# Performance work log

Hardware: AMD Instinct MI355X
Metric: run time of the kernel (lower is better)

The kernel has to match this reference:

```python
import jax, jax.numpy as jnp
import numpy as np

N0, N1, N2 = 100000, 400000, 100000
EU0, EU1, EB1, EB2 = 1600000, 1200000, 800000, 300000
D, H = 64, 64  # layer_dim, hidden
BN_EPS = 1e-5


def _bn(x, g, b):
    # BatchNorm1d in training mode (batch statistics, biased variance)
    m = jnp.mean(x, axis=0)
    v = jnp.mean((x - m) ** 2, axis=0)
    return (x - m) * jax.lax.rsqrt(v + BN_EPS) * g + b


def _mlp(x, W1, b1, g1, be1, W2, b2, g2, be2):
    # Linear -> BN -> ReLU -> Linear -> BN -> ReLU
    h = jax.nn.relu(_bn(x @ W1 + b1, g1, be1))
    return jax.nn.relu(_bn(h @ W2 + b2, g2, be2))


def setup_inputs() -> dict:
    key = jax.random.key(0)
    ks = jax.random.split(key, 16)
    s = 0.1  # weight init scale
    inp = {
        'x0': jax.random.normal(ks[0], (N0, D), jnp.float32),
        'x1': jax.random.normal(ks[1], (N1, D), jnp.float32),
        'x2': jax.random.normal(ks[2], (N2, D), jnp.float32),
        'up_index0': jax.random.randint(ks[3], (2, EU0), 0, N0, jnp.int32),
        'up_index1': jax.random.randint(ks[4], (2, EU1), 0, N1, jnp.int32),
        'bnd_src1': jax.random.randint(ks[5], (EB1,), 0, N0, jnp.int32),
        'bnd_dst1': jax.random.randint(ks[6], (EB1,), 0, N1, jnp.int32),
        'bnd_src2': jax.random.randint(ks[7], (EB2,), 0, N1, jnp.int32),
        'bnd_dst2': jax.random.randint(ks[8], (EB2,), 0, N2, jnp.int32),
        'up_W1': jax.random.normal(ks[9], (3, D, H), jnp.float32) * s,
        'up_b1': jnp.zeros((3, H), jnp.float32),
        'up_g1': jnp.ones((3, H), jnp.float32),
        'up_be1': jnp.zeros((3, H), jnp.float32),
        'up_W2': jax.random.normal(ks[10], (3, H, H), jnp.float32) * s,
        'up_b2': jnp.zeros((3, H), jnp.float32),
        'up_g2': jnp.ones((3, H), jnp.float32),
        'up_be2': jnp.zeros((3, H), jnp.float32),
        'bd_W1': jax.random.normal(ks[11], (3, D, H), jnp.float32) * s,
        'bd_b1': jnp.zeros((3, H), jnp.float32),
        'bd_g1': jnp.ones((3, H), jnp.float32),
        'bd_be1': jnp.zeros((3, H), jnp.float32),
        'bd_W2': jax.random.normal(ks[12], (3, H, H), jnp.float32) * s,
        'bd_b2': jnp.zeros((3, H), jnp.float32),
        'bd_g2': jnp.ones((3, H), jnp.float32),
        'bd_be2': jnp.zeros((3, H), jnp.float32),
        'cmb_W': jax.random.normal(ks[13], (3, 2 * H, H), jnp.float32) * s,
        'cmb_b': jnp.zeros((3, H), jnp.float32),
        'cmb_g': jnp.ones((3, H), jnp.float32),
        'cmb_be': jnp.zeros((3, H), jnp.float32),
        'eps': jnp.zeros((3,), jnp.float32),  # eps1 per dim (eps2 unused in forward)
    }
    return inp


def reference(x0, x1, x2, up_index0, up_index1, bnd_src1, bnd_dst1, bnd_src2, bnd_dst2,
              up_W1, up_b1, up_g1, up_be1, up_W2, up_b2, up_g2, up_be2,
              bd_W1, bd_b1, bd_g1, bd_be1, bd_W2, bd_b2, bd_g2, bd_be2,
              cmb_W, cmb_b, cmb_g, cmb_be, eps):
    seg = jax.ops.segment_sum

    def level(d, x, agg_up, agg_bd):
        z = (1.0 + eps[d]) * x
        out_up = _mlp(agg_up + z, up_W1[d], up_b1[d], up_g1[d], up_be1[d],
                      up_W2[d], up_b2[d], up_g2[d], up_be2[d])
        out_bd = _mlp(agg_bd + z, bd_W1[d], bd_b1[d], bd_g1[d], bd_be1[d],
                      bd_W2[d], bd_b2[d], bd_g2[d], bd_be2[d])
        cat = jnp.concatenate([out_up, out_bd], axis=-1)
        return jax.nn.relu(_bn(cat @ cmb_W[d] + cmb_b[d], cmb_g[d], cmb_be[d]))

    # dim 0: upper adjacency only (no boundaries for nodes)
    agg_up0 = seg(x0[up_index0[0]], up_index0[1], num_segments=N0)
    out0 = level(0, x0, agg_up0, jnp.zeros_like(x0))

    # dim 1: upper adjacency (via 2-cells) + node boundaries (boundary_attr = x0)
    agg_up1 = seg(x1[up_index1[0]], up_index1[1], num_segments=N1)
    agg_bd1 = seg(x0[bnd_src1], bnd_dst1, num_segments=N1)
    out1 = level(1, x1, agg_up1, agg_bd1)

    # dim 2: edge boundaries only (boundary_attr = x1), no upper adjacency
    agg_bd2 = seg(x1[bnd_src2], bnd_dst2, num_segments=N2)
    out2 = level(2, x2, jnp.zeros_like(x2), agg_bd2)

    return (out0, out1, out2)
```

## Files before the change

kernel.cpp:

```cpp
#include <hip/hip_runtime.h>
#include <cstdint>
#include <cstddef>


using bfrag = __attribute__((ext_vector_type(8))) short;
using f32x4 = __attribute__((ext_vector_type(4))) float;

__device__ __forceinline__ unsigned short f2bf(float f) {
    unsigned int u = __float_as_uint(f);
    u += 0x7FFFu + ((u >> 16) & 1u);
    return (unsigned short)(u >> 16);
}
__device__ __forceinline__ float bf2f(unsigned int h) {
    return __uint_as_float(h << 16);
}


__global__ __launch_bounds__(256) void hist_ranged_k(
    const int* __restrict__ d0, const int* __restrict__ d1,
    const int* __restrict__ d2, const int* __restrict__ d3,
    int E0, int E1, int E2, int E3,
    int o0, int o1, int o2, int o3,
    int* __restrict__ cnt, int NT)
{
    const int pass = blockIdx.x & 7;
    const int W = (NT + 7) >> 3;
    const int lo = pass * W;
    int hi = lo + W; if (hi > NT) hi = NT;
    const int ET = E0 + E1 + E2 + E3;
    const int nsub = gridDim.x >> 3;
    for (int e = (blockIdx.x >> 3) * 256 + threadIdx.x; e < ET; e += nsub * 256) {
        int g;
        if (e < E0) g = o0 + d0[e];
        else if (e < E0 + E1) g = o1 + d1[e - E0];
        else if (e < E0 + E1 + E2) g = o2 + d2[e - E0 - E1];
        else g = o3 + d3[e - E0 - E1 - E2];
        if (g >= lo && g < hi) atomicAdd(&cnt[g], 1);
    }
}

__global__ __launch_bounds__(256) void fill_ranged_k(
    const int* __restrict__ s0, const int* __restrict__ d0,
    const int* __restrict__ s1, const int* __restrict__ d1,
    const int* __restrict__ s2, const int* __restrict__ d2,
    const int* __restrict__ s3, const int* __restrict__ d3,
    int E0, int E1, int E2, int E3,
    int o0, int o1, int o2, int o3,
    int* __restrict__ cur, int* __restrict__ esrc, int NT)
{
    const int pass = blockIdx.x & 7;
    const int W = (NT + 7) >> 3;
    const int lo = pass * W;
    int hi = lo + W; if (hi > NT) hi = NT;
    const int ET = E0 + E1 + E2 + E3;
    const int nsub = gridDim.x >> 3;
    for (int e = (blockIdx.x >> 3) * 256 + threadIdx.x; e < ET; e += nsub * 256) {
        int g; const int* sp; int ei;
        if (e < E0) { g = o0 + d0[e]; sp = s0; ei = e; }
        else if (e < E0 + E1) { ei = e - E0; g = o1 + d1[ei]; sp = s1; }
        else if (e < E0 + E1 + E2) { ei = e - E0 - E1; g = o2 + d2[ei]; sp = s2; }
        else { ei = e - E0 - E1 - E2; g = o3 + d3[ei]; sp = s3; }
        if (g >= lo && g < hi) {
            int pos = atomicAdd(&cur[g], 1);
            esrc[pos] = sp[ei];
        }
    }
}

__global__ __launch_bounds__(256) void scanA_k(int* __restrict__ a,
                                               int* __restrict__ bsum, int n) {
    __shared__ int ts[256];
    int tid = threadIdx.x;
    int base = blockIdx.x * 2048 + tid * 8;
    int v[8]; int s = 0;
    #pragma unroll
    for (int i = 0; i < 8; ++i) { v[i] = (base + i < n) ? a[base + i] : 0; s += v[i]; }
    ts[tid] = s;
    __syncthreads();
    for (int off = 1; off < 256; off <<= 1) {
        int t = (tid >= off) ? ts[tid - off] : 0;
        __syncthreads();
        ts[tid] += t;
        __syncthreads();
    }
    int run = ts[tid] - s;
    #pragma unroll
    for (int i = 0; i < 8; ++i) {
        if (base + i < n) { int o = v[i]; a[base + i] = run; run += o; }
    }
    if (tid == 255) bsum[blockIdx.x] = ts[255];
}

__global__ __launch_bounds__(512) void scanB_k(int* __restrict__ bsum, int nb) {
    __shared__ int ls[512];
    int tid = threadIdx.x;
    int v = (tid < nb) ? bsum[tid] : 0;
    ls[tid] = v;
    __syncthreads();
    for (int off = 1; off < 512; off <<= 1) {
        int t = (tid >= off) ? ls[tid - off] : 0;
        __syncthreads();
        ls[tid] += t;
        __syncthreads();
    }
    if (tid < nb) bsum[tid] = ls[tid] - v;
}

__global__ __launch_bounds__(256) void scanC_k(int* __restrict__ a,
                                               const int* __restrict__ bsum, int n) {
    int base = blockIdx.x * 2048 + threadIdx.x * 8;
    int add = bsum[blockIdx.x];
    #pragma unroll
    for (int i = 0; i < 8; ++i)
        if (base + i < n) a[base + i] += add;
}


__global__ __launch_bounds__(256) void wprep_k(
    const float* __restrict__ upW1, const float* __restrict__ upW2,
    const float* __restrict__ bdW1, const float* __restrict__ bdW2,
    const float* __restrict__ cmbW, unsigned short* __restrict__ wT)
{
    int id = blockIdx.x;
    int d = id / 5, j = id % 5;
    const float* src; int K = 64;
    if (j == 0)      src = upW1 + (size_t)d * 4096;
    else if (j == 1) src = upW2 + (size_t)d * 4096;
    else if (j == 2) src = bdW1 + (size_t)d * 4096;
    else if (j == 3) src = bdW2 + (size_t)d * 4096;
    else           { src = cmbW + (size_t)d * 8192; K = 128; }
    unsigned short* dst = wT + (size_t)d * 24576 + (j < 4 ? j * 4096 : 16384);
    for (int e = threadIdx.x; e < K * 64; e += 256) {
        int k = e >> 6, n = e & 63;
        dst[n * K + k] = f2bf(src[e]);
    }
}


struct SegG {
    const int* cur;
    const float* xs; const float* xself;
    const unsigned short* in0; const unsigned short* in1;
    const float* st0; const float* g0; const float* be0;
    const float* st1; const float* g1; const float* be1;
    const unsigned short* wT; const float* bias;
    unsigned short* out; float* ostats;
    int N; int blk0; int eBase; int epsIdx;
};
struct GemmArgs { SegG s[6]; int nseg; const int* esrc; const float* epsP; };

__global__ __launch_bounds__(256) void gemm_bn_multi_k(int mode, GemmArgs A)
{
    __shared__ unsigned short sIn[64][72];
    __shared__ unsigned short sW[64][72];
    __shared__ float sCoef[4][64];
    __shared__ float sBias[64];
    __shared__ float sRedS[4][64];
    __shared__ float sRedQ[4][64];

    int si = 0;
    #pragma unroll
    for (int i = 1; i < 6; ++i)
        if (i < A.nseg && (int)blockIdx.x >= A.s[i].blk0) si = i;
    const SegG S = A.s[si];
    const int* esrc = A.esrc;

    const int tid = threadIdx.x;
    const int row0 = ((int)blockIdx.x - S.blk0) * 64;
    const int N = S.N;
    const float Nf = (float)N;

    if (tid < 64) {
        sBias[tid] = S.bias[tid];
        if (mode >= 1) {
            float s = S.st0[tid], sq = S.st0[64 + tid];
            float m = s / Nf, v = sq / Nf - m * m;
            float a = S.g0[tid] * rsqrtf(v + 1e-5f);
            sCoef[0][tid] = a; sCoef[1][tid] = S.be0[tid] - a * m;
        }
    } else if (tid < 128 && mode == 2) {
        int k = tid - 64;
        float s = S.st1[k], sq = S.st1[64 + k];
        float m = s / Nf, v = sq / Nf - m * m;
        float a = S.g1[k] * rsqrtf(v + 1e-5f);
        sCoef[2][k] = a; sCoef[3][k] = S.be1[k] - a * m;
    }
    const float sx = (mode == 0) ? (1.0f + A.epsP[S.epsIdx]) : 0.f;
    __syncthreads();

    f32x4 acc[4] = {};
    const int K = (mode == 2) ? 128 : 64;
    const int nch = (mode == 2) ? 2 : 1;
    const int wv = tid >> 6, l = tid & 63, l15 = l & 15, quad = l >> 4;

    for (int ch = 0; ch < nch; ++ch) {
        if (ch) __syncthreads();
        if (mode == 0) {
            const int grp = tid >> 4, lane = tid & 15;
            const int r0g = row0 + grp * 4;
            float ax[4], ay[4], az[4], aw[4];
            int beg[4], deg[4];
            #pragma unroll
            for (int rr = 0; rr < 4; ++rr) {
                int gr = r0g + rr;
                float4 xv = {0.f, 0.f, 0.f, 0.f};
                if (gr < N)
                    xv = *(const float4*)(S.xself + (size_t)gr * 64 + lane * 4);
                ax[rr] = sx * xv.x; ay[rr] = sx * xv.y;
                az[rr] = sx * xv.z; aw[rr] = sx * xv.w;
                int b = 0, d = 0;
                if (gr < N && S.cur) {
                    b = (gr == 0) ? S.eBase : S.cur[gr - 1];
                    d = S.cur[gr] - b;
                }
                beg[rr] = b; deg[rr] = d;
            }
            #pragma unroll
            for (int rr = 0; rr < 4; ++rr) {
                for (int base = 0; base < deg[rr]; base += 16) {
                    int take = deg[rr] - base; if (take > 16) take = 16;
                    int idxl = 0;
                    if (lane < take) idxl = esrc[beg[rr] + base + lane];
                    for (int j0 = 0; j0 < take; j0 += 4) {
                        float4 v0 = {0,0,0,0}, v1 = {0,0,0,0};
                        float4 v2 = {0,0,0,0}, v3 = {0,0,0,0};
                        int si2 = __shfl(idxl, j0, 16);
                        v0 = *(const float4*)(S.xs + (size_t)si2 * 64 + lane * 4);
                        if (j0 + 1 < take) {
                            si2 = __shfl(idxl, j0 + 1, 16);
                            v1 = *(const float4*)(S.xs + (size_t)si2 * 64 + lane * 4);
                        }
                        if (j0 + 2 < take) {
                            si2 = __shfl(idxl, j0 + 2, 16);
                            v2 = *(const float4*)(S.xs + (size_t)si2 * 64 + lane * 4);
                        }
                        if (j0 + 3 < take) {
                            si2 = __shfl(idxl, j0 + 3, 16);
                            v3 = *(const float4*)(S.xs + (size_t)si2 * 64 + lane * 4);
                        }
                        ax[rr] += (v0.x + v1.x) + (v2.x + v3.x);
                        ay[rr] += (v0.y + v1.y) + (v2.y + v3.y);
                        az[rr] += (v0.z + v1.z) + (v2.z + v3.z);
                        aw[rr] += (v0.w + v1.w) + (v2.w + v3.w);
                    }
                }
                ushort4 pk;
                pk.x = f2bf(ax[rr]); pk.y = f2bf(ay[rr]);
                pk.z = f2bf(az[rr]); pk.w = f2bf(aw[rr]);
                *(ushort4*)&sIn[grp * 4 + rr][lane * 4] = pk;
            }
        } else {
            const unsigned short* base = ch ? S.in1 : S.in0;
            const int ci = ch * 2;
            #pragma unroll
            for (int it = 0; it < 2; ++it) {
                int id = tid + it * 256;
                int r = id >> 3, c8 = id & 7;
                int gr = row0 + r;
                uint4 pk = {0u, 0u, 0u, 0u};
                if (gr < N) {
                    uint4 raw = *(const uint4*)(base + (size_t)gr * 64 + c8 * 8);
                    unsigned int rw[4] = {raw.x, raw.y, raw.z, raw.w};
                    unsigned int ow[4];
                    #pragma unroll
                    for (int q2 = 0; q2 < 4; ++q2) {
                        int col = c8 * 8 + q2 * 2;
                        float v0 = fmaxf(fmaf(sCoef[ci][col], bf2f(rw[q2] & 0xFFFFu),
                                              sCoef[ci + 1][col]), 0.f);
                        float v1 = fmaxf(fmaf(sCoef[ci][col + 1], bf2f(rw[q2] >> 16),
                                              sCoef[ci + 1][col + 1]), 0.f);
                        ow[q2] = (unsigned int)f2bf(v0) | ((unsigned int)f2bf(v1) << 16);
                    }
                    pk.x = ow[0]; pk.y = ow[1]; pk.z = ow[2]; pk.w = ow[3];
                }
                *(uint4*)&sIn[r][c8 * 8] = pk;
            }
        }
        #pragma unroll
        for (int it = 0; it < 2; ++it) {
            int id = tid + it * 256;
            int nr = id >> 3, c8 = id & 7;
            uint4 w = *(const uint4*)(S.wT + (size_t)nr * K + ch * 64 + c8 * 8);
            *(uint4*)&sW[nr][c8 * 8] = w;
        }
        __syncthreads();
        bfrag a0 = *(const bfrag*)&sIn[16 * wv + l15][quad * 8];
        bfrag a1 = *(const bfrag*)&sIn[16 * wv + l15][32 + quad * 8];
        #pragma unroll
        for (int c = 0; c < 4; ++c) {
            bfrag b0 = *(const bfrag*)&sW[16 * c + l15][quad * 8];
            bfrag b1 = *(const bfrag*)&sW[16 * c + l15][32 + quad * 8];
            acc[c] = __builtin_amdgcn_mfma_f32_16x16x32_bf16(a0, b0, acc[c], 0, 0, 0);
            acc[c] = __builtin_amdgcn_mfma_f32_16x16x32_bf16(a1, b1, acc[c], 0, 0, 0);
        }
    }

    float psv[4], pqv[4];
    #pragma unroll
    for (int c = 0; c < 4; ++c) {
        int col = 16 * c + l15;
        float b = sBias[col];
        float ps = 0.f, pq = 0.f;
        #pragma unroll
        for (int r = 0; r < 4; ++r) {
            int grow = row0 + 16 * wv + quad * 4 + r;
            if (grow < N) {
                float v = acc[c][r] + b;
                S.out[(size_t)grow * 64 + col] = f2bf(v);
                ps += v; pq += v * v;
            }
        }
        psv[c] = ps; pqv[c] = pq;
    }
    #pragma unroll
    for (int c = 0; c < 4; ++c) {
        float ps = psv[c], pq = pqv[c];
        ps += __shfl_xor(ps, 16, 64); pq += __shfl_xor(pq, 16, 64);
        ps += __shfl_xor(ps, 32, 64); pq += __shfl_xor(pq, 32, 64);
        if (l < 16) { sRedS[wv][16 * c + l] = ps; sRedQ[wv][16 * c + l] = pq; }
    }
    __syncthreads();
    if (tid < 64) {
        float s = sRedS[0][tid] + sRedS[1][tid] + sRedS[2][tid] + sRedS[3][tid];
        float q = sRedQ[0][tid] + sRedQ[1][tid] + sRedQ[2][tid] + sRedQ[3][tid];
        unsafeAtomicAdd(&S.ostats[tid], s);
        unsafeAtomicAdd(&S.ostats[64 + tid], q);
    }
}


struct SegA {
    const unsigned short* in; const float* st; const float* g; const float* be;
    float* out; int N; int blk0;
};
struct ApplyArgs { SegA s[2]; int nseg; };

__global__ __launch_bounds__(256) void bn_relu_apply_multi_k(ApplyArgs A)
{
    __shared__ float sa[64], sc[64];
    int si = 0;
    if (A.nseg > 1 && (int)blockIdx.x >= A.s[1].blk0) si = 1;
    const SegA S = A.s[si];
    int tid = threadIdx.x;
    if (tid < 64) {
        float s = S.st[tid], sq = S.st[64 + tid];
        float m = s / (float)S.N, v = sq / (float)S.N - m * m;
        float a = S.g[tid] * rsqrtf(v + 1e-5f);
        sa[tid] = a; sc[tid] = S.be[tid] - a * m;
    }
    __syncthreads();
    int idx = ((int)blockIdx.x - S.blk0) * 256 + tid;
    if (idx < S.N * 8) {
        int r = idx >> 3, c8 = idx & 7;
        uint4 raw = *(const uint4*)(S.in + (size_t)r * 64 + c8 * 8);
        unsigned int rw[4] = {raw.x, raw.y, raw.z, raw.w};
        float o[8];
        #pragma unroll
        for (int q = 0; q < 4; ++q) {
            int col = c8 * 8 + q * 2;
            o[q * 2 + 0] = fmaxf(fmaf(sa[col + 0], bf2f(rw[q] & 0xFFFFu), sc[col + 0]), 0.f);
            o[q * 2 + 1] = fmaxf(fmaf(sa[col + 1], bf2f(rw[q] >> 16), sc[col + 1]), 0.f);
        }
        float4 o0 = {o[0], o[1], o[2], o[3]}, o1 = {o[4], o[5], o[6], o[7]};
        *(float4*)(S.out + (size_t)r * 64 + c8 * 8) = o0;
        *(float4*)(S.out + (size_t)r * 64 + c8 * 8 + 4) = o1;
    }
}

extern "C" void kernel_launch(void* const* d_in, const int* in_sizes, int n_in,
                              void* d_out, int out_size, void* d_ws, size_t ws_size,
                              hipStream_t stream) {
    (void)n_in; (void)out_size; (void)ws_size;
    const float* x0 = (const float*)d_in[0];
    const float* x1 = (const float*)d_in[1];
    const float* x2 = (const float*)d_in[2];
    const int* up_index0 = (const int*)d_in[3];
    const int* up_index1 = (const int*)d_in[4];
    const int* bnd_src1  = (const int*)d_in[5];
    const int* bnd_dst1  = (const int*)d_in[6];
    const int* bnd_src2  = (const int*)d_in[7];
    const int* bnd_dst2  = (const int*)d_in[8];
    const float* up_W1 = (const float*)d_in[9];
    const float* up_b1 = (const float*)d_in[10];
    const float* up_g1 = (const float*)d_in[11];
    const float* up_be1= (const float*)d_in[12];
    const float* up_W2 = (const float*)d_in[13];
    const float* up_b2 = (const float*)d_in[14];
    const float* up_g2 = (const float*)d_in[15];
    const float* up_be2= (const float*)d_in[16];
    const float* bd_W1 = (const float*)d_in[17];
    const float* bd_b1 = (const float*)d_in[18];
    const float* bd_g1 = (const float*)d_in[19];
    const float* bd_be1= (const float*)d_in[20];
    const float* bd_W2 = (const float*)d_in[21];
    const float* bd_b2 = (const float*)d_in[22];
    const float* bd_g2 = (const float*)d_in[23];
    const float* bd_be2= (const float*)d_in[24];
    const float* cmb_W = (const float*)d_in[25];
    const float* cmb_b = (const float*)d_in[26];
    const float* cmb_g = (const float*)d_in[27];
    const float* cmb_be= (const float*)d_in[28];
    const float* epsP  = (const float*)d_in[29];

    const int EU0 = in_sizes[3] / 2, EU1 = in_sizes[4] / 2;
    const int EB1 = in_sizes[5],     EB2 = in_sizes[7];
    const int n0 = in_sizes[0] / 64, n1 = in_sizes[1] / 64, n2 = in_sizes[2] / 64;
    const int nMax02 = (n0 > n2) ? n0 : n2;

    float* outP = (float*)d_out;

    unsigned short* bufU = (unsigned short*)d_ws;
    unsigned short* bufB = bufU + (size_t)n1 * 64;
    float* stats = (float*)(bufB + (size_t)nMax02 * 64);
    int*   bsum  = (int*)(stats + 15 * 128);
    unsigned short* wT = (unsigned short*)(bsum + 1024);

    const int NT  = n0 + 2 * n1 + n2;
    const int ETT = EU0 + EU1 + EB1 + EB2;
    const int oU0 = 0, oU1 = n0, oB1 = n0 + n1, oB2 = n0 + 2 * n1;
    const int eU0 = 0, eU1 = EU0, eB1 = EU0 + EU1, eB2 = EU0 + EU1 + EB1;
    int* curAll  = (int*)(outP + (size_t)(n0 + n1) * 64);
    int* esrcAll = curAll + NT;

    unsigned short* hU0 = bufB;
    unsigned short* hB0 = (unsigned short*)outP;
    unsigned short* hU2 = (unsigned short*)outP + (size_t)n0 * 64;
    unsigned short* hU1 = bufU;
    unsigned short* hB1 = (unsigned short*)(outP + (size_t)n0 * 64);
    unsigned short* hB2 = (unsigned short*)(outP + (size_t)n0 * 64) + (size_t)n1 * 64;

    hipMemsetAsync(stats, 0, 15 * 128 * sizeof(float), stream);
    wprep_k<<<15, 256, 0, stream>>>(up_W1, up_W2, bd_W1, bd_W2, cmb_W, wT);

    hipMemsetAsync(curAll, 0, (size_t)NT * sizeof(int), stream);
    hist_ranged_k<<<2048, 256, 0, stream>>>(
        up_index0 + EU0, up_index1 + EU1, bnd_dst1, bnd_dst2,
        EU0, EU1, EB1, EB2, oU0, oU1, oB1, oB2, curAll, NT);
    int nbScan = (NT + 2047) / 2048;
    scanA_k<<<nbScan, 256, 0, stream>>>(curAll, bsum, NT);
    scanB_k<<<1, 512, 0, stream>>>(bsum, nbScan);
    scanC_k<<<nbScan, 256, 0, stream>>>(curAll, bsum, NT);
    fill_ranged_k<<<2048, 256, 0, stream>>>(
        up_index0, up_index0 + EU0, up_index1, up_index1 + EU1,
        bnd_src1, bnd_dst1, bnd_src2, bnd_dst2,
        EU0, EU1, EB1, EB2, oU0, oU1, oB1, oB2, curAll, esrcAll, NT);

    auto S  = [&](int d, int i) { return stats + (size_t)(d * 5 + i) * 128; };
    auto WTf = [&](int d, int j) { return wT + (size_t)d * 24576 + (j < 4 ? j * 4096 : 16384); };

    const int nb0 = (n0 + 63) / 64, nb1 = (n1 + 63) / 64, nb2 = (n2 + 63) / 64;

    {
        GemmArgs A{}; A.nseg = 6; A.esrc = esrcAll; A.epsP = epsP;
        auto& s = A.s;
        s[0] = { curAll + oU0, x0, x0, nullptr, nullptr,
                 nullptr, nullptr, nullptr, nullptr, nullptr, nullptr,
                 WTf(0,0), up_b1 + 0, hU0, S(0,0), n0, 0, eU0, 0 };
        s[1] = { nullptr, nullptr, x0, nullptr, nullptr,
                 nullptr, nullptr, nullptr, nullptr, nullptr, nullptr,
                 WTf(0,2), bd_b1 + 0, hB0, S(0,2), n0, nb0, 0, 0 };
        s[2] = { curAll + oU1, x1, x1, nullptr, nullptr,
                 nullptr, nullptr, nullptr, nullptr, nullptr, nullptr,
                 WTf(1,0), up_b1 + 64, hU1, S(1,0), n1, 2*nb0, eU1, 1 };
        s[3] = { curAll + oB1, x0, x1, nullptr, nullptr,
                 nullptr, nullptr, nullptr, nullptr, nullptr, nullptr,
                 WTf(1,2), bd_b1 + 64, hB1, S(1,2), n1, 2*nb0 + nb1, eB1, 1 };
        s[4] = { nullptr, nullptr, x2, nullptr, nullptr,
                 nullptr, nullptr, nullptr, nullptr, nullptr, nullptr,
                 WTf(2,0), up_b1 + 128, hU2, S(2,0), n2, 2*nb0 + 2*nb1, 0, 2 };
        s[5] = { curAll + oB2, x1, x2, nullptr, nullptr,
                 nullptr, nullptr, nullptr, nullptr, nullptr, nullptr,
                 WTf(2,2), bd_b1 + 128, hB2, S(2,2), n2, 2*nb0 + 2*nb1 + nb2, eB2, 2 };
        gemm_bn_multi_k<<<2*nb0 + 2*nb1 + 2*nb2, 256, 0, stream>>>(0, A);
    }

    {
        GemmArgs A{}; A.nseg = 6; A.esrc = nullptr; A.epsP = epsP;
        auto& s = A.s;
        s[0] = { nullptr, nullptr, nullptr, hU0, nullptr,
                 S(0,0), up_g1 + 0, up_be1 + 0, nullptr, nullptr, nullptr,
                 WTf(0,1), up_b2 + 0, hU0, S(0,1), n0, 0, 0, 0 };
        s[1] = { nullptr, nullptr, nullptr, hB0, nullptr,
                 S(0,2), bd_g1 + 0, bd_be1 + 0, nullptr, nullptr, nullptr,
                 WTf(0,3), bd_b2 + 0, hB0, S(0,3), n0, nb0, 0, 0 };
        s[2] = { nullptr, nullptr, nullptr, hU1, nullptr,
                 S(1,0), up_g1 + 64, up_be1 + 64, nullptr, nullptr, nullptr,
                 WTf(1,1), up_b2 + 64, hU1, S(1,1), n1, 2*nb0, 0, 0 };
        s[3] = { nullptr, nullptr, nullptr, hB1, nullptr,
                 S(1,2), bd_g1 + 64, bd_be1 + 64, nullptr, nullptr, nullptr,
                 WTf(1,3), bd_b2 + 64, hB1, S(1,3), n1, 2*nb0 + nb1, 0, 0 };
        s[4] = { nullptr, nullptr, nullptr, hU2, nullptr,
                 S(2,0), up_g1 + 128, up_be1 + 128, nullptr, nullptr, nullptr,
                 WTf(2,1), up_b2 + 128, hU2, S(2,1), n2, 2*nb0 + 2*nb1, 0, 0 };
        s[5] = { nullptr, nullptr, nullptr, hB2, nullptr,
                 S(2,2), bd_g1 + 128, bd_be1 + 128, nullptr, nullptr, nullptr,
                 WTf(2,3), bd_b2 + 128, hB2, S(2,3), n2, 2*nb0 + 2*nb1 + nb2, 0, 0 };
        gemm_bn_multi_k<<<2*nb0 + 2*nb1 + 2*nb2, 256, 0, stream>>>(1, A);
    }

    {
        GemmArgs A{}; A.nseg = 3; A.esrc = nullptr; A.epsP = epsP;
        auto& s = A.s;
        s[0] = { nullptr, nullptr, nullptr, hU0, hB0,
                 S(0,1), up_g2 + 0, up_be2 + 0, S(0,3), bd_g2 + 0, bd_be2 + 0,
                 WTf(0,4), cmb_b + 0, hU0, S(0,4), n0, 0, 0, 0 };
        s[1] = { nullptr, nullptr, nullptr, hU1, hB1,
                 S(1,1), up_g2 + 64, up_be2 + 64, S(1,3), bd_g2 + 64, bd_be2 + 64,
                 WTf(1,4), cmb_b + 64, hU1, S(1,4), n1, nb0, 0, 0 };
        s[2] = { nullptr, nullptr, nullptr, hU2, hB2,
                 S(2,1), up_g2 + 128, up_be2 + 128, S(2,3), bd_g2 + 128, bd_be2 + 128,
                 WTf(2,4), cmb_b + 128, hU2, S(2,4), n2, nb0 + nb1, 0, 0 };
        gemm_bn_multi_k<<<nb0 + nb1 + nb2, 256, 0, stream>>>(2, A);
    }

    {
        ApplyArgs A{}; A.nseg = 1;
        A.s[0] = { hU2, S(2,4), cmb_g + 128, cmb_be + 128,
                   outP + (size_t)(n0 + n1) * 64, n2, 0 };
        bn_relu_apply_multi_k<<<(n2 * 8 + 255) / 256, 256, 0, stream>>>(A);
    }
    {
        ApplyArgs A{}; A.nseg = 2;
        int ab0 = (n0 * 8 + 255) / 256;
        A.s[0] = { hU0, S(0,4), cmb_g + 0, cmb_be + 0, outP, n0, 0 };
        A.s[1] = { hU1, S(1,4), cmb_g + 64, cmb_be + 64,
                   outP + (size_t)n0 * 64, n1, ab0 };
        bn_relu_apply_multi_k<<<ab0 + (n1 * 8 + 255) / 256, 256, 0, stream>>>(A);
    }
}
```

Before: 1.733 ms.

## Fuse up and boundary first-layer GEMMs into one pair kernel per row block

The first stage now runs one block per 64-row tile that gathers both the upper-adjacency and the boundary aggregates, and runs both first-layer GEMMs with BN-stat accumulation. Before, up and boundary were separate blocks. Fusing them loads x_self once per tile and halves the block count, at the cost of more registers per thread for two sets of accumulators. It also switches the intermediate and final output stores to nontemporal stores.

Result: faster. 1.590 ms (-8.3%).

```diff
diff --git a/kernel.cpp b/kernel.cpp
--- a/kernel.cpp
+++ b/kernel.cpp
@@ -5,6 +5,8 @@
 
 using bfrag = __attribute__((ext_vector_type(8))) short;
 using f32x4 = __attribute__((ext_vector_type(4))) float;
+using u4v   = __attribute__((ext_vector_type(4))) unsigned int;
+using f4v   = __attribute__((ext_vector_type(4))) float;
 
 __device__ __forceinline__ unsigned short f2bf(float f) {
     unsigned int u = __float_as_uint(f);
@@ -137,17 +139,199 @@
 }
 
 
+struct SegP {
+    const int* curU; const int* curB;
+    const float* xsU; const float* xsB;
+    const float* xself;
+    const unsigned short* wTU; const unsigned short* wTB;
+    const float* biasU; const float* biasB;
+    unsigned short* outU; unsigned short* outB;
+    float* statsU; float* statsB;
+    int N; int blk0; int eBaseU; int eBaseB; int epsIdx;
+};
+struct PairArgs { SegP s[3]; const int* esrc; const float* epsP; };
+
+__global__ __launch_bounds__(256) void gemm_pair_k(PairArgs A)
+{
+    __shared__ unsigned short sIn[64][72];
+    __shared__ unsigned short sW[64][72];
+    __shared__ float sBias[64];
+    __shared__ float sRedS[4][64];
+    __shared__ float sRedQ[4][64];
+
+    int si = 0;
+    if ((int)blockIdx.x >= A.s[1].blk0) si = 1;
+    if ((int)blockIdx.x >= A.s[2].blk0) si = 2;
+    const SegP S = A.s[si];
+    const int* esrc = A.esrc;
+
+    const int tid = threadIdx.x;
+    const int row0 = ((int)blockIdx.x - S.blk0) * 64;
+    const int N = S.N;
+    const float sx = 1.0f + A.epsP[S.epsIdx];
+
+    const int wv = tid >> 6, l = tid & 63, l15 = l & 15, quad = l >> 4;
+    const int grp = tid >> 4, lane = tid & 15;
+    const int r0g = row0 + grp * 4;
+
+    float axU[4], ayU[4], azU[4], awU[4];
+    float axB[4], ayB[4], azB[4], awB[4];
+    #pragma unroll
+    for (int rr = 0; rr < 4; ++rr) {
+        int gr = r0g + rr;
+        float4 xv = {0.f, 0.f, 0.f, 0.f};
+        if (gr < N)
+            xv = *(const float4*)(S.xself + (size_t)gr * 64 + lane * 4);
+        axU[rr] = sx * xv.x; ayU[rr] = sx * xv.y;
+        azU[rr] = sx * xv.z; awU[rr] = sx * xv.w;
+        axB[rr] = axU[rr]; ayB[rr] = ayU[rr];
+        azB[rr] = azU[rr]; awB[rr] = awU[rr];
+    }
+
+    auto gatherAcc = [&](const int* cur, int eBase, const float* xs,
+                         float (&ax)[4], float (&ay)[4], float (&az)[4],
+                         float (&aw)[4]) {
+        if (!cur) return;
+        int beg[4], deg[4];
+        #pragma unroll
+        for (int rr = 0; rr < 4; ++rr) {
+            int gr = r0g + rr; int b = 0, d = 0;
+            if (gr < N) {
+                b = (gr == 0) ? eBase : cur[gr - 1];
+                d = cur[gr] - b;
+            }
+            beg[rr] = b; deg[rr] = d;
+        }
+        #pragma unroll
+        for (int rr = 0; rr < 4; ++rr) {
+            for (int base = 0; base < deg[rr]; base += 16) {
+                int take = deg[rr] - base; if (take > 16) take = 16;
+                int idxl = 0;
+                if (lane < take) idxl = esrc[beg[rr] + base + lane];
+                for (int j0 = 0; j0 < take; j0 += 4) {
+                    float4 v0 = {0,0,0,0}, v1 = {0,0,0,0};
+                    float4 v2 = {0,0,0,0}, v3 = {0,0,0,0};
+                    int si2 = __shfl(idxl, j0, 16);
+                    v0 = *(const float4*)(xs + (size_t)si2 * 64 + lane * 4);
+                    if (j0 + 1 < take) {
+                        si2 = __shfl(idxl, j0 + 1, 16);
+                        v1 = *(const float4*)(xs + (size_t)si2 * 64 + lane * 4);
+                    }
+                    if (j0 + 2 < take) {
+                        si2 = __shfl(idxl, j0 + 2, 16);
+                        v2 = *(const float4*)(xs + (size_t)si2 * 64 + lane * 4);
+                    }
+                    if (j0 + 3 < take) {
+                        si2 = __shfl(idxl, j0 + 3, 16);
+                        v3 = *(const float4*)(xs + (size_t)si2 * 64 + lane * 4);
+                    }
+                    ax[rr] += (v0.x + v1.x) + (v2.x + v3.x);
+                    ay[rr] += (v0.y + v1.y) + (v2.y + v3.y);
+                    az[rr] += (v0.z + v1.z) + (v2.z + v3.z);
+                    aw[rr] += (v0.w + v1.w) + (v2.w + v3.w);
+                }
+            }
+        }
+    };
+    gatherAcc(S.curU, S.eBaseU, S.xsU, axU, ayU, azU, awU);
+    gatherAcc(S.curB, S.eBaseB, S.xsB, axB, ayB, azB, awB);
+
+    #pragma unroll
+    for (int br = 0; br < 2; ++br) {
+        if (br) __syncthreads();
+        const unsigned short* wTp = br ? S.wTB : S.wTU;
+        const float* biasp = br ? S.biasB : S.biasU;
+        unsigned short* outp = br ? S.outB : S.outU;
+        float* statsp = br ? S.statsB : S.statsU;
+
+        if (tid < 64) sBias[tid] = biasp[tid];
+        {
+            ushort4 pk;
+            #pragma unroll
+            for (int rr = 0; rr < 4; ++rr) {
+                float x_ = br ? axB[rr] : axU[rr];
+                float y_ = br ? ayB[rr] : ayU[rr];
+                float z_ = br ? azB[rr] : azU[rr];
+                float w_ = br ? awB[rr] : awU[rr];
+                pk.x = f2bf(x_); pk.y = f2bf(y_);
+                pk.z = f2bf(z_); pk.w = f2bf(w_);
+                *(ushort4*)&sIn[grp * 4 + rr][lane * 4] = pk;
+            }
+        }
+        #pragma unroll
+        for (int it = 0; it < 2; ++it) {
+            int id = tid + it * 256;
+            int nr = id >> 3, c8 = id & 7;
+            uint4 w = *(const uint4*)(wTp + (size_t)nr * 64 + c8 * 8);
+            *(uint4*)&sW[nr][c8 * 8] = w;
+        }
+        __syncthreads();
+
+        bfrag a0 = *(const bfrag*)&sIn[16 * wv + l15][quad * 8];
+        bfrag a1 = *(const bfrag*)&sIn[16 * wv + l15][32 + quad * 8];
+        f32x4 acc[4] = {};
+        #pragma unroll
+        for (int c = 0; c < 4; ++c) {
+            bfrag b0 = *(const bfrag*)&sW[16 * c + l15][quad * 8];
+            bfrag b1 = *(const bfrag*)&sW[16 * c + l15][32 + quad * 8];
+            acc[c] = __builtin_amdgcn_mfma_f32_16x16x32_bf16(a0, b0, acc[c], 0, 0, 0);
+            acc[c] = __builtin_amdgcn_mfma_f32_16x16x32_bf16(a1, b1, acc[c], 0, 0, 0);
+        }
+        __syncthreads();
+
+        float psv[4], pqv[4];
+        #pragma unroll
+        for (int c = 0; c < 4; ++c) {
+            int col = 16 * c + l15;
+            float b = sBias[col];
+            float ps = 0.f, pq = 0.f;
+            #pragma unroll
+            for (int r4 = 0; r4 < 4; ++r4) {
+                int lr = 16 * wv + quad * 4 + r4;
+                float v = acc[c][r4] + b;
+                sIn[lr][col] = f2bf(v);
+                if (row0 + lr < N) { ps += v; pq += v * v; }
+            }
+            psv[c] = ps; pqv[c] = pq;
+        }
+        #pragma unroll
+        for (int c = 0; c < 4; ++c) {
+            float ps = psv[c], pq = pqv[c];
+            ps += __shfl_xor(ps, 16, 64); pq += __shfl_xor(pq, 16, 64);
+            ps += __shfl_xor(ps, 32, 64); pq += __shfl_xor(pq, 32, 64);
+            if (l < 16) { sRedS[wv][16 * c + l] = ps; sRedQ[wv][16 * c + l] = pq; }
+        }
+        __syncthreads();
+
+        #pragma unroll
+        for (int it = 0; it < 2; ++it) {
+            int id = tid + it * 256;
+            int r = id >> 3, c8 = id & 7;
+            if (row0 + r < N) {
+                u4v w = *(const u4v*)&sIn[r][c8 * 8];
+                __builtin_nontemporal_store(
+                    w, (u4v*)(outp + (size_t)(row0 + r) * 64 + c8 * 8));
+            }
+        }
+        if (tid < 64) {
+            float s = sRedS[0][tid] + sRedS[1][tid] + sRedS[2][tid] + sRedS[3][tid];
+            float q = sRedQ[0][tid] + sRedQ[1][tid] + sRedQ[2][tid] + sRedQ[3][tid];
+            unsafeAtomicAdd(&statsp[tid], s);
+            unsafeAtomicAdd(&statsp[64 + tid], q);
+        }
+    }
+}
+
+
 struct SegG {
-    const int* cur;
-    const float* xs; const float* xself;
     const unsigned short* in0; const unsigned short* in1;
     const float* st0; const float* g0; const float* be0;
     const float* st1; const float* g1; const float* be1;
     const unsigned short* wT; const float* bias;
     unsigned short* out; float* ostats;
-    int N; int blk0; int eBase; int epsIdx;
+    int N; int blk0;
 };
-struct GemmArgs { SegG s[6]; int nseg; const int* esrc; const float* epsP; };
+struct GemmArgs { SegG s[6]; int nseg; };
 
 __global__ __launch_bounds__(256) void gemm_bn_multi_k(int mode, GemmArgs A)
 {
@@ -163,7 +347,6 @@
     for (int i = 1; i < 6; ++i)
         if (i < A.nseg && (int)blockIdx.x >= A.s[i].blk0) si = i;
     const SegG S = A.s[si];
-    const int* esrc = A.esrc;
 
     const int tid = threadIdx.x;
     const int row0 = ((int)blockIdx.x - S.blk0) * 64;
@@ -172,12 +355,10 @@
 
     if (tid < 64) {
         sBias[tid] = S.bias[tid];
-        if (mode >= 1) {
-            float s = S.st0[tid], sq = S.st0[64 + tid];
-            float m = s / Nf, v = sq / Nf - m * m;
-            float a = S.g0[tid] * rsqrtf(v + 1e-5f);
-            sCoef[0][tid] = a; sCoef[1][tid] = S.be0[tid] - a * m;
-        }
+        float s = S.st0[tid], sq = S.st0[64 + tid];
+        float m = s / Nf, v = sq / Nf - m * m;
+        float a = S.g0[tid] * rsqrtf(v + 1e-5f);
+        sCoef[0][tid] = a; sCoef[1][tid] = S.be0[tid] - a * m;
     } else if (tid < 128 && mode == 2) {
         int k = tid - 64;
         float s = S.st1[k], sq = S.st1[64 + k];
@@ -185,7 +366,6 @@
         float a = S.g1[k] * rsqrtf(v + 1e-5f);
         sCoef[2][k] = a; sCoef[3][k] = S.be1[k] - a * m;
     }
-    const float sx = (mode == 0) ? (1.0f + A.epsP[S.epsIdx]) : 0.f;
     __syncthreads();
 
     f32x4 acc[4] = {};
@@ -195,86 +375,30 @@
 
     for (int ch = 0; ch < nch; ++ch) {
         if (ch) __syncthreads();
-        if (mode == 0) {
-            const int grp = tid >> 4, lane = tid & 15;
-            const int r0g = row0 + grp * 4;
-            float ax[4], ay[4], az[4], aw[4];
-            int beg[4], deg[4];
-            #pragma unroll
-            for (int rr = 0; rr < 4; ++rr) {
-                int gr = r0g + rr;
-                float4 xv = {0.f, 0.f, 0.f, 0.f};
-                if (gr < N)
-                    xv = *(const float4*)(S.xself + (size_t)gr * 64 + lane * 4);
-                ax[rr] = sx * xv.x; ay[rr] = sx * xv.y;
-                az[rr] = sx * xv.z; aw[rr] = sx * xv.w;
-                int b = 0, d = 0;
-                if (gr < N && S.cur) {
-                    b = (gr == 0) ? S.eBase : S.cur[gr - 1];
-                    d = S.cur[gr] - b;
+        const unsigned short* base = ch ? S.in1 : S.in0;
+        const int ci = ch * 2;
+        #pragma unroll
+        for (int it = 0; it < 2; ++it) {
+            int id = tid + it * 256;
+            int r = id >> 3, c8 = id & 7;
+            int gr = row0 + r;
+            uint4 pk = {0u, 0u, 0u, 0u};
+            if (gr < N) {
+                uint4 raw = *(const uint4*)(base + (size_t)gr * 64 + c8 * 8);
+                unsigned int rw[4] = {raw.x, raw.y, raw.z, raw.w};
+                unsigned int ow[4];
+                #pragma unroll
+                for (int q2 = 0; q2 < 4; ++q2) {
+                    int col = c8 * 8 + q2 * 2;
+                    float v0 = fmaxf(fmaf(sCoef[ci][col], bf2f(rw[q2] & 0xFFFFu),
+                                          sCoef[ci + 1][col]), 0.f);
+                    float v1 = fmaxf(fmaf(sCoef[ci][col + 1], bf2f(rw[q2] >> 16),
+                                          sCoef[ci + 1][col + 1]), 0.f);
+                    ow[q2] = (unsigned int)f2bf(v0) | ((unsigned int)f2bf(v1) << 16);
                 }
-                beg[rr] = b; deg[rr] = d;
+                pk.x = ow[0]; pk.y = ow[1]; pk.z = ow[2]; pk.w = ow[3];
             }
-            #pragma unroll
-            for (int rr = 0; rr < 4; ++rr) {
-                for (int base = 0; base < deg[rr]; base += 16) {
-                    int take = deg[rr] - base; if (take > 16) take = 16;
-                    int idxl = 0;
-                    if (lane < take) idxl = esrc[beg[rr] + base + lane];
-                    for (int j0 = 0; j0 < take; j0 += 4) {
-                        float4 v0 = {0,0,0,0}, v1 = {0,0,0,0};
-                        float4 v2 = {0,0,0,0}, v3 = {0,0,0,0};
-                        int si2 = __shfl(idxl, j0, 16);
-                        v0 = *(const float4*)(S.xs + (size_t)si2 * 64 + lane * 4);
-                        if (j0 + 1 < take) {
-                            si2 = __shfl(idxl, j0 + 1, 16);
-                            v1 = *(const float4*)(S.xs + (size_t)si2 * 64 + lane * 4);
-                        }
-                        if (j0 + 2 < take) {
-                            si2 = __shfl(idxl, j0 + 2, 16);
-                            v2 = *(const float4*)(S.xs + (size_t)si2 * 64 + lane * 4);
-                        }
-                        if (j0 + 3 < take) {
-                            si2 = __shfl(idxl, j0 + 3, 16);
-                            v3 = *(const float4*)(S.xs + (size_t)si2 * 64 + lane * 4);
-                        }
-                        ax[rr] += (v0.x + v1.x) + (v2.x + v3.x);
-                        ay[rr] += (v0.y + v1.y) + (v2.y + v3.y);
-                        az[rr] += (v0.z + v1.z) + (v2.z + v3.z);
-                        aw[rr] += (v0.w + v1.w) + (v2.w + v3.w);
-                    }
-                }
-                ushort4 pk;
-                pk.x = f2bf(ax[rr]); pk.y = f2bf(ay[rr]);
-                pk.z = f2bf(az[rr]); pk.w = f2bf(aw[rr]);
-                *(ushort4*)&sIn[grp * 4 + rr][lane * 4] = pk;
-            }
-        } else {
-            const unsigned short* base = ch ? S.in1 : S.in0;
-            const int ci = ch * 2;
-            #pragma unroll
-            for (int it = 0; it < 2; ++it) {
-                int id = tid + it * 256;
-                int r = id >> 3, c8 = id & 7;
-                int gr = row0 + r;
-                uint4 pk = {0u, 0u, 0u, 0u};
-                if (gr < N) {
-                    uint4 raw = *(const uint4*)(base + (size_t)gr * 64 + c8 * 8);
-                    unsigned int rw[4] = {raw.x, raw.y, raw.z, raw.w};
-                    unsigned int ow[4];
-                    #pragma unroll
-                    for (int q2 = 0; q2 < 4; ++q2) {
-                        int col = c8 * 8 + q2 * 2;
-                        float v0 = fmaxf(fmaf(sCoef[ci][col], bf2f(rw[q2] & 0xFFFFu),
-                                              sCoef[ci + 1][col]), 0.f);
-                        float v1 = fmaxf(fmaf(sCoef[ci][col + 1], bf2f(rw[q2] >> 16),
-                                              sCoef[ci + 1][col + 1]), 0.f);
-                        ow[q2] = (unsigned int)f2bf(v0) | ((unsigned int)f2bf(v1) << 16);
-                    }
-                    pk.x = ow[0]; pk.y = ow[1]; pk.z = ow[2]; pk.w = ow[3];
-                }
-                *(uint4*)&sIn[r][c8 * 8] = pk;
-            }
+            *(uint4*)&sIn[r][c8 * 8] = pk;
         }
         #pragma unroll
         for (int it = 0; it < 2; ++it) {
@@ -361,9 +485,9 @@
             o[q * 2 + 0] = fmaxf(fmaf(sa[col + 0], bf2f(rw[q] & 0xFFFFu), sc[col + 0]), 0.f);
             o[q * 2 + 1] = fmaxf(fmaf(sa[col + 1], bf2f(rw[q] >> 16), sc[col + 1]), 0.f);
         }
-        float4 o0 = {o[0], o[1], o[2], o[3]}, o1 = {o[4], o[5], o[6], o[7]};
-        *(float4*)(S.out + (size_t)r * 64 + c8 * 8) = o0;
-        *(float4*)(S.out + (size_t)r * 64 + c8 * 8 + 4) = o1;
+        f4v o0 = {o[0], o[1], o[2], o[3]}, o1 = {o[4], o[5], o[6], o[7]};
+        __builtin_nontemporal_store(o0, (f4v*)(S.out + (size_t)r * 64 + c8 * 8));
+        __builtin_nontemporal_store(o1, (f4v*)(S.out + (size_t)r * 64 + c8 * 8 + 4));
     }
 }
 
@@ -416,7 +540,6 @@
     unsigned short* wT = (unsigned short*)(bsum + 1024);
 
     const int NT  = n0 + 2 * n1 + n2;
-    const int ETT = EU0 + EU1 + EB1 + EB2;
     const int oU0 = 0, oU1 = n0, oB1 = n0 + n1, oB2 = n0 + 2 * n1;
     const int eU0 = 0, eU1 = EU0, eB1 = EU0 + EU1, eB2 = EU0 + EU1 + EB1;
     int* curAll  = (int*)(outP + (size_t)(n0 + n1) * 64);
@@ -451,65 +574,55 @@
     const int nb0 = (n0 + 63) / 64, nb1 = (n1 + 63) / 64, nb2 = (n2 + 63) / 64;
 
     {
-        GemmArgs A{}; A.nseg = 6; A.esrc = esrcAll; A.epsP = epsP;
+        PairArgs A{}; A.esrc = esrcAll; A.epsP = epsP;
+        A.s[0] = { curAll + oU0, nullptr, x0, nullptr, x0,
+                   WTf(0,0), WTf(0,2), up_b1 + 0, bd_b1 + 0,
+                   hU0, hB0, S(0,0), S(0,2), n0, 0, eU0, 0, 0 };
+        A.s[1] = { curAll + oU1, curAll + oB1, x1, x0, x1,
+                   WTf(1,0), WTf(1,2), up_b1 + 64, bd_b1 + 64,
+                   hU1, hB1, S(1,0), S(1,2), n1, nb0, eU1, eB1, 1 };
+        A.s[2] = { nullptr, curAll + oB2, nullptr, x1, x2,
+                   WTf(2,0), WTf(2,2), up_b1 + 128, bd_b1 + 128,
+                   hU2, hB2, S(2,0), S(2,2), n2, nb0 + nb1, 0, eB2, 2 };
+        gemm_pair_k<<<nb0 + nb1 + nb2, 256, 0, stream>>>(A);
+    }
+
+    {
+        GemmArgs A{}; A.nseg = 6;
         auto& s = A.s;
-        s[0] = { curAll + oU0, x0, x0, nullptr, nullptr,
-                 nullptr, nullptr, nullptr, nullptr, nullptr, nullptr,
-                 WTf(0,0), up_b1 + 0, hU0, S(0,0), n0, 0, eU0, 0 };
-        s[1] = { nullptr, nullptr, x0, nullptr, nullptr,
-                 nullptr, nullptr, nullptr, nullptr, nullptr, nullptr,
-                 WTf(0,2), bd_b1 + 0, hB0, S(0,2), n0, nb0, 0, 0 };
-        s[2] = { curAll + oU1, x1, x1, nullptr, nullptr,
-                 nullptr, nullptr, nullptr, nullptr, nullptr, nullptr,
-                 WTf(1,0), up_b1 + 64, hU1, S(1,0), n1, 2*nb0, eU1, 1 };
-        s[3] = { curAll + oB1, x0, x1, nullptr, nullptr,
-                 nullptr, nullptr, nullptr, nullptr, nullptr, nullptr,
-                 WTf(1,2), bd_b1 + 64, hB1, S(1,2), n1, 2*nb0 + nb1, eB1, 1 };
-        s[4] = { nullptr, nullptr, x2, nullptr, nullptr,
-                 nullptr, nullptr, nullptr, nullptr, nullptr, nullptr,
-                 WTf(2,0), up_b1 + 128, hU2, S(2,0), n2, 2*nb0 + 2*nb1, 0, 2 };
-        s[5] = { curAll + oB2, x1, x2, nullptr, nullptr,
-                 nullptr, nullptr, nullptr, nullptr, nullptr, nullptr,
-                 WTf(2,2), bd_b1 + 128, hB2, S(2,2), n2, 2*nb0 + 2*nb1 + nb2, eB2, 2 };
-        gemm_bn_multi_k<<<2*nb0 + 2*nb1 + 2*nb2, 256, 0, stream>>>(0, A);
+        s[0] = { hU0, nullptr, S(0,0), up_g1 + 0, up_be1 + 0,
+                 nullptr, nullptr, nullptr,
+                 WTf(0,1), up_b2 + 0, hU0, S(0,1), n0, 0 };
+        s[1] = { hB0, nullptr, S(0,2), bd_g1 + 0, bd_be1 + 0,
+                 nullptr, nullptr, nullptr,
+                 WTf(0,3), bd_b2 + 0, hB0, S(0,3), n0, nb0 };
+        s[2] = { hU1, nullptr, S(1,0), up_g1 + 64, up_be1 + 64,
+                 nullptr, nullptr, nullptr,
+                 WTf(1,1), up_b2 + 64, hU1, S(1,1), n1, 2*nb0 };
+        s[3] = { hB1, nullptr, S(1,2), bd_g1 + 64, bd_be1 + 64,
+                 nullptr, nullptr, nullptr,
+                 WTf(1,3), bd_b2 + 64, hB1, S(1,3), n1, 2*nb0 + nb1 };
+        s[4] = { hU2, nullptr, S(2,0), up_g1 + 128, up_be1 + 128,
+                 nullptr, nullptr, nullptr,
+                 WTf(2,1), up_b2 + 128, hU2, S(2,1), n2, 2*nb0 + 2*nb1 };
+        s[5] = { hB2, nullptr, S(2,2), bd_g1 + 128, bd_be1 + 128,
+                 nullptr, nullptr, nullptr,
+                 WTf(2,3), bd_b2 + 128, hB2, S(2,3), n2, 2*nb0 + 2*nb1 + nb2 };
+        gemm_bn_multi_k<<<2*nb0 + 2*nb1 + 2*nb2, 256, 0, stream>>>(1, A);
     }
 
     {
-        GemmArgs A{}; A.nseg = 6; A.esrc = nullptr; A.epsP = epsP;
+        GemmArgs A{}; A.nseg = 3;
         auto& s = A.s;
-        s[0] = { nullptr, nullptr, nullptr, hU0, nullptr,
-                 S(0,0), up_g1 + 0, up_be1 + 0, nullptr, nullptr, nullptr,
-                 WTf(0,1), up_b2 + 0, hU0, S(0,1), n0, 0, 0, 0 };
-        s[1] = { nullptr, nullptr, nullptr, hB0, nullptr,
-                 S(0,2), bd_g1 + 0, bd_be1 + 0, nullptr, nullptr, nullptr,
-                 WTf(0,3), bd_b2 + 0, hB0, S(0,3), n0, nb0, 0, 0 };
-        s[2] = { nullptr, nullptr, nullptr, hU1, nullptr,
-                 S(1,0), up_g1 + 64, up_be1 + 64, nullptr, nullptr, nullptr,
-                 WTf(1,1), up_b2 + 64, hU1, S(1,1), n1, 2*nb0, 0, 0 };
-        s[3] = { nullptr, nullptr, nullptr, hB1, nullptr,
-                 S(1,2), bd_g1 + 64, bd_be1 + 64, nullptr, nullptr, nullptr,
-                 WTf(1,3), bd_b2 + 64, hB1, S(1,3), n1, 2*nb0 + nb1, 0, 0 };
-        s[4] = { nullptr, nullptr, nullptr, hU2, nullptr,
-                 S(2,0), up_g1 + 128, up_be1 + 128, nullptr, nullptr, nullptr,
-                 WTf(2,1), up_b2 + 128, hU2, S(2,1), n2, 2*nb0 + 2*nb1, 0, 0 };
-        s[5] = { nullptr, nullptr, nullptr, hB2, nullptr,
-                 S(2,2), bd_g1 + 128, bd_be1 + 128, nullptr, nullptr, nullptr,
-                 WTf(2,3), bd_b2 + 128, hB2, S(2,3), n2, 2*nb0 + 2*nb1 + nb2, 0, 0 };
-        gemm_bn_multi_k<<<2*nb0 + 2*nb1 + 2*nb2, 256, 0, stream>>>(1, A);
-    }
-
-    {
-        GemmArgs A{}; A.nseg = 3; A.esrc = nullptr; A.epsP = epsP;
-        auto& s = A.s;
-        s[0] = { nullptr, nullptr, nullptr, hU0, hB0,
-                 S(0,1), up_g2 + 0, up_be2 + 0, S(0,3), bd_g2 + 0, bd_be2 + 0,
-                 WTf(0,4), cmb_b + 0, hU0, S(0,4), n0, 0, 0, 0 };
-        s[1] = { nullptr, nullptr, nullptr, hU1, hB1,
-                 S(1,1), up_g2 + 64, up_be2 + 64, S(1,3), bd_g2 + 64, bd_be2 + 64,
-                 WTf(1,4), cmb_b + 64, hU1, S(1,4), n1, nb0, 0, 0 };
-        s[2] = { nullptr, nullptr, nullptr, hU2, hB2,
-                 S(2,1), up_g2 + 128, up_be2 + 128, S(2,3), bd_g2 + 128, bd_be2 + 128,
-                 WTf(2,4), cmb_b + 128, hU2, S(2,4), n2, nb0 + nb1, 0, 0 };
+        s[0] = { hU0, hB0, S(0,1), up_g2 + 0, up_be2 + 0,
+                 S(0,3), bd_g2 + 0, bd_be2 + 0,
+                 WTf(0,4), cmb_b + 0, hU0, S(0,4), n0, 0 };
+        s[1] = { hU1, hB1, S(1,1), up_g2 + 64, up_be2 + 64,
+                 S(1,3), bd_g2 + 64, bd_be2 + 64,
+                 WTf(1,4), cmb_b + 64, hU1, S(1,4), n1, nb0 };
+        s[2] = { hU2, hB2, S(2,1), up_g2 + 128, up_be2 + 128,
+                 S(2,3), bd_g2 + 128, bd_be2 + 128,
+                 WTf(2,4), cmb_b + 128, hU2, S(2,4), n2, nb0 + nb1 };
         gemm_bn_multi_k<<<nb0 + nb1 + nb2, 256, 0, stream>>>(2, A);
     }
 
```
